# Performance work log

Hardware: AMD Instinct MI355X
Metric: run time of the kernel (lower is better)

Reference implementation:

```python
import jax, jax.numpy as jnp
import numpy as np

H = 12          # num attention heads
D_HEAD = 64     # head size (768 / 12)
P = 2           # power-law exponent
C = 5.0         # score shift
EPS = 1e-10


def setup_inputs() -> dict:
    key = jax.random.key(0)
    ks = jax.random.split(key, 8)
    B, S, Dm = 32, 512, 768
    scale = 1.0 / np.sqrt(Dm)
    return {
        "hidden_states": jax.random.normal(ks[0], (B, S, Dm), dtype=jnp.float32),
        "attention_mask": jnp.ones((B, 1, 1, S), dtype=jnp.float32),
        "Wq": jax.random.normal(ks[1], (Dm, Dm), dtype=jnp.float32) * scale,
        "bq": jnp.zeros((Dm,), dtype=jnp.float32),
        "Wk": jax.random.normal(ks[2], (Dm, Dm), dtype=jnp.float32) * scale,
        "bk": jnp.zeros((Dm,), dtype=jnp.float32),
        "Wv": jax.random.normal(ks[3], (Dm, Dm), dtype=jnp.float32) * scale,
        "bv": jnp.zeros((Dm,), dtype=jnp.float32),
    }


def _heads(x, B, S):
    # [B, S, H*d] -> [B, H, S, d]
    return x.reshape(B, S, H, D_HEAD).transpose(0, 2, 1, 3)


def reference(hidden_states, attention_mask, Wq, bq, Wk, bk, Wv, bv):
    B, S, Dm = hidden_states.shape
    q = _heads(hidden_states @ Wq + bq, B, S)
    k = _heads(hidden_states @ Wk + bk, B, S)
    v = _heads(hidden_states @ Wv + bv, B, S)

    inv_sqrt_d = 1.0 / (np.sqrt(D_HEAD) + 1e-10)
    scores = jnp.einsum("bhqd,bhkd->bhqk", q, k) * inv_sqrt_d  # [B,H,S,S]

    # Power-law attention (Powerformer, distill=0 branch)
    probs = jnp.power(scores + C, P)
    probs = probs / (jnp.sum(probs, axis=-1, keepdims=True) + EPS)
    probs = probs * attention_mask  # mask multiplied after normalization

    ctx = jnp.einsum("bhqk,bhkd->bhqd", probs, v)  # [B,H,S,d]
    ctx = ctx.transpose(0, 2, 1, 3).reshape(B, S, Dm)
    return ctx
```

## Files before the change

### kernel.cpp

```cpp
#include <hip/hip_runtime.h>

typedef __attribute__((ext_vector_type(8))) _Float16 half8;
typedef __attribute__((ext_vector_type(4))) _Float16 half4;
typedef __attribute__((ext_vector_type(4))) float f32x4;

#define MFMA_K32(a, b, c) __builtin_amdgcn_mfma_f32_16x16x32_f16((a), (b), (c), 0, 0, 0)
#define MFMA_K16(a, b, c) __builtin_amdgcn_mfma_f32_16x16x16f16((a), (b), (c), 0, 0, 0)

__device__ inline void async16(const _Float16* g, _Float16* l) {
    __builtin_amdgcn_global_load_lds(
        (const __attribute__((address_space(1))) void*)g,
        (__attribute__((address_space(3))) void*)l, 16, 0, 0);
}


__global__ __launch_bounds__(256) void prep_kernel(
    const float* __restrict__ X, _Float16* __restrict__ Xh,
    const float* __restrict__ W0, const float* __restrict__ W1,
    const float* __restrict__ W2,
    _Float16* __restrict__ T0, _Float16* __restrict__ T1,
    _Float16* __restrict__ T2)
{
    __shared__ float tile[32][33];
    int bid = blockIdx.x;
    if (bid < 6144) {
        size_t idx = ((size_t)bid * 256 + threadIdx.x) * 8;
        float4 a = *(const float4*)(X + idx);
        float4 c = *(const float4*)(X + idx + 4);
        half8 hv;
        hv[0] = (_Float16)a.x; hv[1] = (_Float16)a.y;
        hv[2] = (_Float16)a.z; hv[3] = (_Float16)a.w;
        hv[4] = (_Float16)c.x; hv[5] = (_Float16)c.y;
        hv[6] = (_Float16)c.z; hv[7] = (_Float16)c.w;
        *(half8*)(Xh + idx) = hv;
    } else {
        int id = bid - 6144;
        int z = id / 576; id -= z * 576;
        int n0 = (id / 24) * 32, k0 = (id % 24) * 32;
        const float* W = (z == 0) ? W0 : (z == 1) ? W1 : W2;
        _Float16* T = (z == 0) ? T0 : (z == 1) ? T1 : T2;
        int tx = threadIdx.x & 31, ty = threadIdx.x >> 5;
#pragma unroll
        for (int r = 0; r < 4; ++r)
            tile[ty + 8 * r][tx] = W[(size_t)(k0 + ty + 8 * r) * 768 + n0 + tx];
        __syncthreads();
#pragma unroll
        for (int r = 0; r < 4; ++r)
            T[(size_t)(n0 + ty + 8 * r) * 768 + k0 + tx] =
                (_Float16)tile[tx][ty + 8 * r];
    }
}

__global__ __launch_bounds__(256) void qkv_gemm(
    const _Float16* __restrict__ Xh,
    const _Float16* __restrict__ W0, const _Float16* __restrict__ W1,
    const _Float16* __restrict__ W2,
    const float* __restrict__ b0, const float* __restrict__ b1,
    const float* __restrict__ b2,
    const float* __restrict__ mask,
    _Float16* __restrict__ Qo, _Float16* __restrict__ Ko,
    _Float16* __restrict__ Vo)
{
    int z = blockIdx.y / 6;
    int n0 = (blockIdx.y % 6) * 128;
    int m0 = blockIdx.x * 128;
    const _Float16* Wt = (z == 0) ? W0 : (z == 1) ? W1 : W2;
    const float* bias = (z == 0) ? b0 : (z == 1) ? b1 : b2;

    __shared__ __attribute__((aligned(16))) _Float16 As[128 * 64];
    __shared__ __attribute__((aligned(16))) _Float16 Bs[128 * 64];

    int t = threadIdx.x;
    int wave = t >> 6, lane = t & 63, quad = lane >> 4, l16 = lane & 15;
    int wm = (wave & 1) * 64, wn = (wave >> 1) * 64;

    int srow = t >> 3;
    int sg = (t & 7) ^ (srow & 7);

    const _Float16* gA = Xh + (size_t)(m0 + srow) * 768 + sg * 8;
    const _Float16* gB = Wt + (size_t)(n0 + srow) * 768 + sg * 8;
    _Float16* lA = As + t * 8;
    _Float16* lB = Bs + t * 8;

    const _Float16* Pa = (z == 2) ? As : Bs;
    const _Float16* Pb = (z == 2) ? Bs : As;

    f32x4 acc[4][4] = {};

    for (int k0 = 0; k0 < 768; k0 += 64) {
#pragma unroll
        for (int q = 0; q < 4; ++q) {
            async16(gA + (size_t)q * 32 * 768 + k0, lA + q * 2048);
            async16(gB + (size_t)q * 32 * 768 + k0, lB + q * 2048);
        }
        __syncthreads();
#pragma unroll
        for (int ks = 0; ks < 2; ++ks) {
            half8 af[4], bf[4];
#pragma unroll
            for (int i = 0; i < 4; ++i) {
                int row = wm + i * 16 + l16;
                af[i] = *(const half8*)&Pa[row * 64 +
                                           (((ks << 2) + quad) ^ (row & 7)) * 8];
            }
#pragma unroll
            for (int j = 0; j < 4; ++j) {
                int row = wn + j * 16 + l16;
                bf[j] = *(const half8*)&Pb[row * 64 +
                                           (((ks << 2) + quad) ^ (row & 7)) * 8];
            }
#pragma unroll
            for (int i = 0; i < 4; ++i)
#pragma unroll
                for (int j = 0; j < 4; ++j)
                    acc[i][j] = MFMA_K32(af[i], bf[j], acc[i][j]);
        }
        __syncthreads();
    }

    if (z != 2) {
#pragma unroll
        for (int i = 0; i < 4; ++i) {
            int nbase = n0 + wm + i * 16 + quad * 4;
            int hh = nbase >> 6, dbase = nbase & 63;
            float4 bv4 = *(const float4*)&bias[nbase];
#pragma unroll
            for (int j = 0; j < 4; ++j) {
                int token = m0 + wn + j * 16 + l16;
                int bb = token >> 9, s = token & 511;
                half4 pk;
                if (z == 0) {
#pragma unroll
                    for (int r = 0; r < 4; ++r)
                        pk[r] = (_Float16)((acc[i][j][r] + ((const float*)&bv4)[r]) * 0.125f);
                } else {
#pragma unroll
                    for (int r = 0; r < 4; ++r)
                        pk[r] = (_Float16)(acc[i][j][r] + ((const float*)&bv4)[r]);
                }
                size_t off = (((size_t)(bb * 12 + hh)) * 512 + s) * 64 + dbase;
                if (z == 0) *(half4*)&Qo[off] = pk;
                else        *(half4*)&Ko[off] = pk;
            }
        }
    } else {
        float mk[4][4];
#pragma unroll
        for (int i = 0; i < 4; ++i) {
            int mbase = m0 + wm + i * 16 + quad * 4;
            int bb = mbase >> 9, s = mbase & 511;
#pragma unroll
            for (int r = 0; r < 4; ++r)
                mk[i][r] = mask[(size_t)bb * 512 + s + r];
        }
#pragma unroll
        for (int j = 0; j < 4; ++j) {
            int n = n0 + wn + j * 16 + l16;
            float bv = bias[n];
            int hh = n >> 6, d = n & 63;
#pragma unroll
            for (int i = 0; i < 4; ++i) {
                int mbase = m0 + wm + i * 16 + quad * 4;
                int bb = mbase >> 9, s = mbase & 511;
                half4 pk;
#pragma unroll
                for (int r = 0; r < 4; ++r)
                    pk[r] = (_Float16)((acc[i][j][r] + bv) * mk[i][r]);
                size_t off = (((size_t)(bb * 12 + hh)) * 64 + d) * 512 + s;
                *(half4*)&Vo[off] = pk;
            }
        }
    }
}

__global__ __launch_bounds__(256) void attn_kernel(
    const _Float16* __restrict__ Q, const _Float16* __restrict__ K,
    const _Float16* __restrict__ Vt, float* __restrict__ out)
{
    __shared__ __attribute__((aligned(16))) _Float16 Ks[2][64 * 88];
    __shared__ __attribute__((aligned(16))) _Float16 Vs[2][64 * 88];

    int t = threadIdx.x;
    int wave = t >> 6, lane = t & 63, quad = lane >> 4, l16 = lane & 15;
    int h = blockIdx.y, b = blockIdx.z;
    size_t bh = (size_t)b * 12 + h;
    const _Float16* Qp = Q + bh * (512 * 64);
    const _Float16* Kp = K + bh * (512 * 64);
    const _Float16* Vp = Vt + bh * (64 * 512);
    int qbase = blockIdx.x * 256 + wave * 64;

    half8 qf[4][2];
#pragma unroll
    for (int i = 0; i < 4; ++i)
#pragma unroll
        for (int ks = 0; ks < 2; ++ks)
            qf[i][ks] = *(const half8*)(Qp + (size_t)(qbase + i * 16 + l16) * 64 +
                                        ks * 32 + quad * 8);

    f32x4 ctx[4][4] = {};
    f32x4 rsum[4] = {};
    const half4 ones = {(_Float16)1.f, (_Float16)1.f, (_Float16)1.f, (_Float16)1.f};

    int srow = t >> 2, spart = (t & 3) * 16;
    const _Float16* kgb = Kp + (size_t)srow * 64 + spart;
    const _Float16* vgb = Vp + (size_t)srow * 512 + spart;

    half8 ka0 = *(const half8*)(kgb);
    half8 ka1 = *(const half8*)(kgb + 8);
    half8 va0 = *(const half8*)(vgb);
    half8 va1 = *(const half8*)(vgb + 8);
    *(half8*)&Ks[0][srow * 88 + spart] = ka0;
    *(half8*)&Ks[0][srow * 88 + spart + 8] = ka1;
    *(half8*)&Vs[0][srow * 88 + spart] = va0;
    *(half8*)&Vs[0][srow * 88 + spart + 8] = va1;
    __syncthreads();

    for (int kt = 0; kt < 8; ++kt) {
        int c = kt & 1;
        if (kt < 7) {
            size_t ko = (size_t)(kt + 1) * 64;
            ka0 = *(const half8*)(kgb + ko * 64);
            ka1 = *(const half8*)(kgb + ko * 64 + 8);
            va0 = *(const half8*)(vgb + ko);
            va1 = *(const half8*)(vgb + ko + 8);
        }

        __builtin_amdgcn_s_setprio(1);
#pragma unroll
        for (int kb = 0; kb < 4; ++kb) {
            half8 kf0 = *(const half8*)&Ks[c][(kb * 16 + l16) * 88 + quad * 8];
            half8 kf1 = *(const half8*)&Ks[c][(kb * 16 + l16) * 88 + 32 + quad * 8];
            f32x4 sc[4];
#pragma unroll
            for (int i = 0; i < 4; ++i) {
                f32x4 s0 = {0.f, 0.f, 0.f, 0.f};
                s0 = MFMA_K32(kf0, qf[i][0], s0);
                sc[i] = MFMA_K32(kf1, qf[i][1], s0);
            }
            half4 pA[4];
#pragma unroll
            for (int i = 0; i < 4; ++i) {
#pragma unroll
                for (int r = 0; r < 4; ++r) {
                    float s = sc[i][r] + 5.0f;
                    pA[i][r] = (_Float16)(s * s);
                }
            }
#pragma unroll
            for (int i = 0; i < 4; ++i)
                rsum[i] = MFMA_K16(pA[i], ones, rsum[i]);
#pragma unroll
            for (int n = 0; n < 4; ++n) {
                half4 vf = *(const half4*)&Vs[c][(n * 16 + l16) * 88 + kb * 16 + quad * 4];
#pragma unroll
                for (int i = 0; i < 4; ++i)
                    ctx[i][n] = MFMA_K16(pA[i], vf, ctx[i][n]);
            }
        }
        __builtin_amdgcn_s_setprio(0);

        if (kt < 7) {
            *(half8*)&Ks[1 - c][srow * 88 + spart] = ka0;
            *(half8*)&Ks[1 - c][srow * 88 + spart + 8] = ka1;
            *(half8*)&Vs[1 - c][srow * 88 + spart] = va0;
            *(half8*)&Vs[1 - c][srow * 88 + spart + 8] = va1;
        }
        __syncthreads();
    }

#pragma unroll
    for (int i = 0; i < 4; ++i) {
        f32x4 inv;
#pragma unroll
        for (int r = 0; r < 4; ++r)
            inv[r] = 1.0f / (rsum[i][r] + 1e-10f);
#pragma unroll
        for (int n = 0; n < 4; ++n)
#pragma unroll
            for (int r = 0; r < 4; ++r) {
                int q = qbase + i * 16 + quad * 4 + r;
                int d = n * 16 + l16;
                out[((size_t)b * 512 + q) * 768 + h * 64 + d] =
                    ctx[i][n][r] * inv[r];
            }
    }
}

extern "C" void kernel_launch(void* const* d_in, const int* in_sizes, int n_in,
                              void* d_out, int out_size, void* d_ws, size_t ws_size,
                              hipStream_t stream)
{
    const float* hs   = (const float*)d_in[0];
    const float* mask = (const float*)d_in[1];
    const float* Wq   = (const float*)d_in[2];
    const float* bq   = (const float*)d_in[3];
    const float* Wk   = (const float*)d_in[4];
    const float* bk   = (const float*)d_in[5];
    const float* Wv   = (const float*)d_in[6];
    const float* bv   = (const float*)d_in[7];
    float* out = (float*)d_out;

    char* ws = (char*)d_ws;
    _Float16* Wtq = (_Float16*)ws;
    _Float16* Wtk = Wtq + 768 * 768;
    _Float16* Wtv = Wtk + 768 * 768;
    _Float16* Qb  = Wtv + 768 * 768;
    _Float16* Kb  = Qb + 16384 * 768;
    _Float16* Vb  = Kb + 16384 * 768;
    _Float16* Xh = (_Float16*)d_out;

    prep_kernel<<<dim3(7872), 256, 0, stream>>>(hs, Xh, Wq, Wk, Wv,
                                                Wtq, Wtk, Wtv);
    qkv_gemm<<<dim3(128, 18), 256, 0, stream>>>(Xh, Wtq, Wtk, Wtv,
                                                bq, bk, bv, mask, Qb, Kb, Vb);
    attn_kernel<<<dim3(2, 12, 32), 256, 0, stream>>>(Qb, Kb, Vb, out);
}
```

Before: 234.1 us.

## Double-buffer QKV GEMM LDS tiles with K=32 steps and async prefetch

Restructures the QKV projection GEMM main loop to use two LDS buffers of 128x32 tiles, issuing async global-to-LDS loads for the next K slice while MFMAs run on the current one. This aims to hide global load latency behind compute and cut one barrier per iteration. It also drops the XOR swizzle in favour of a plain 32-element row layout, which may bring LDS bank conflicts back on the fragment reads. The iteration count doubles to 24 with a smaller K per step.

```diff
diff --git a/kernel.cpp b/kernel.cpp
--- a/kernel.cpp
+++ b/kernel.cpp
@@ -67,56 +67,53 @@
     const _Float16* Wt = (z == 0) ? W0 : (z == 1) ? W1 : W2;
     const float* bias = (z == 0) ? b0 : (z == 1) ? b1 : b2;
 
-    __shared__ __attribute__((aligned(16))) _Float16 As[128 * 64];
-    __shared__ __attribute__((aligned(16))) _Float16 Bs[128 * 64];
+    __shared__ __attribute__((aligned(16))) _Float16 As[2 * 4096];
+    __shared__ __attribute__((aligned(16))) _Float16 Bs[2 * 4096];
 
     int t = threadIdx.x;
     int wave = t >> 6, lane = t & 63, quad = lane >> 4, l16 = lane & 15;
     int wm = (wave & 1) * 64, wn = (wave >> 1) * 64;
 
-    int srow = t >> 3;
-    int sg = (t & 7) ^ (srow & 7);
-
-    const _Float16* gA = Xh + (size_t)(m0 + srow) * 768 + sg * 8;
-    const _Float16* gB = Wt + (size_t)(n0 + srow) * 768 + sg * 8;
+    int tr4 = t >> 2, tc4 = t & 3;
+    const _Float16* gA = Xh + (size_t)(m0 + tr4) * 768 + tc4 * 8;
+    const _Float16* gB = Wt + (size_t)(n0 + tr4) * 768 + tc4 * 8;
     _Float16* lA = As + t * 8;
     _Float16* lB = Bs + t * 8;
 
+#define STAGE(buf, k0v) do {                                          \
+        async16(gA + (k0v),              lA + (buf) * 4096);          \
+        async16(gA + 64 * 768 + (k0v),   lA + (buf) * 4096 + 2048);   \
+        async16(gB + (k0v),              lB + (buf) * 4096);          \
+        async16(gB + 64 * 768 + (k0v),   lB + (buf) * 4096 + 2048); } while (0)
+
     const _Float16* Pa = (z == 2) ? As : Bs;
     const _Float16* Pb = (z == 2) ? Bs : As;
 
     f32x4 acc[4][4] = {};
 
-    for (int k0 = 0; k0 < 768; k0 += 64) {
-#pragma unroll
-        for (int q = 0; q < 4; ++q) {
-            async16(gA + (size_t)q * 32 * 768 + k0, lA + q * 2048);
-            async16(gB + (size_t)q * 32 * 768 + k0, lB + q * 2048);
-        }
+    STAGE(0, 0);
+    __syncthreads();
+
+    for (int kt = 0; kt < 24; ++kt) {
+        int c = kt & 1;
+        if (kt < 23) STAGE(c ^ 1, (kt + 1) * 32);
+
+        half8 af[4], bf[4];
+#pragma unroll
+        for (int i = 0; i < 4; ++i)
+            af[i] = *(const half8*)&Pa[c * 4096 + (wm + i * 16 + l16) * 32 + quad * 8];
+#pragma unroll
+        for (int j = 0; j < 4; ++j)
+            bf[j] = *(const half8*)&Pb[c * 4096 + (wn + j * 16 + l16) * 32 + quad * 8];
+#pragma unroll
+        for (int i = 0; i < 4; ++i)
+#pragma unroll
+            for (int j = 0; j < 4; ++j)
+                acc[i][j] = MFMA_K32(af[i], bf[j], acc[i][j]);
+
         __syncthreads();
-#pragma unroll
-        for (int ks = 0; ks < 2; ++ks) {
-            half8 af[4], bf[4];
-#pragma unroll
-            for (int i = 0; i < 4; ++i) {
-                int row = wm + i * 16 + l16;
-                af[i] = *(const half8*)&Pa[row * 64 +
-                                           (((ks << 2) + quad) ^ (row & 7)) * 8];
-            }
-#pragma unroll
-            for (int j = 0; j < 4; ++j) {
-                int row = wn + j * 16 + l16;
-                bf[j] = *(const half8*)&Pb[row * 64 +
-                                           (((ks << 2) + quad) ^ (row & 7)) * 8];
-            }
-#pragma unroll
-            for (int i = 0; i < 4; ++i)
-#pragma unroll
-                for (int j = 0; j < 4; ++j)
-                    acc[i][j] = MFMA_K32(af[i], bf[j], acc[i][j]);
-        }
-        __syncthreads();
-    }
+    }
+#undef STAGE
 
     if (z != 2) {
 #pragma unroll
```

After: 246.7 us. 1.05x slower.

## Double-buffer QKV GEMM LDS tiles with async prefetch of next k-tile

Applied to the files above, without the earlier changes.

The QKV projection GEMM now keeps two LDS buffers for the A and B tiles and issues the asynchronous global-to-LDS loads for the next k-tile before computing on the current one. It waits with a partial vmcnt so only the current tile's loads must have landed. This is meant to hide global load latency behind the MFMA work. In exchange LDS use doubles to 64 KB per block, which may lower occupancy, and the code relies on hand-placed waitcnt and barrier ordering.

```diff
diff --git a/kernel.cpp b/kernel.cpp
--- a/kernel.cpp
+++ b/kernel.cpp
@@ -67,8 +67,8 @@
     const _Float16* Wt = (z == 0) ? W0 : (z == 1) ? W1 : W2;
     const float* bias = (z == 0) ? b0 : (z == 1) ? b1 : b2;
 
-    __shared__ __attribute__((aligned(16))) _Float16 As[128 * 64];
-    __shared__ __attribute__((aligned(16))) _Float16 Bs[128 * 64];
+    __shared__ __attribute__((aligned(16))) _Float16 As[2 * 8192];
+    __shared__ __attribute__((aligned(16))) _Float16 Bs[2 * 8192];
 
     int t = threadIdx.x;
     int wave = t >> 6, lane = t & 63, quad = lane >> 4, l16 = lane & 15;
@@ -82,32 +82,60 @@
     _Float16* lA = As + t * 8;
     _Float16* lB = Bs + t * 8;
 
+#define STAGE(buf, k0v) do {                                                   \
+        async16(gA,                    lA + (buf) * 8192);                     \
+        async16(gA + (size_t)1 * 32 * 768 + (k0v) - (k0v) + (k0v), lA + (buf) * 8192 + 2048); \
+        async16(gA + (size_t)2 * 32 * 768 + (k0v), lA + (buf) * 8192 + 4096);  \
+        async16(gA + (size_t)3 * 32 * 768 + (k0v), lA + (buf) * 8192 + 6144);  \
+        async16(gB + (k0v),            lB + (buf) * 8192);                     \
+        async16(gB + (size_t)1 * 32 * 768 + (k0v), lB + (buf) * 8192 + 2048);  \
+        async16(gB + (size_t)2 * 32 * 768 + (k0v), lB + (buf) * 8192 + 4096);  \
+        async16(gB + (size_t)3 * 32 * 768 + (k0v), lB + (buf) * 8192 + 6144); } while (0)
+#undef STAGE
+#define STAGE(buf, k0v) do {                                                   \
+        async16(gA + (k0v),                        lA + (buf) * 8192);         \
+        async16(gA + (size_t)1 * 32 * 768 + (k0v), lA + (buf) * 8192 + 2048);  \
+        async16(gA + (size_t)2 * 32 * 768 + (k0v), lA + (buf) * 8192 + 4096);  \
+        async16(gA + (size_t)3 * 32 * 768 + (k0v), lA + (buf) * 8192 + 6144);  \
+        async16(gB + (k0v),                        lB + (buf) * 8192);         \
+        async16(gB + (size_t)1 * 32 * 768 + (k0v), lB + (buf) * 8192 + 2048);  \
+        async16(gB + (size_t)2 * 32 * 768 + (k0v), lB + (buf) * 8192 + 4096);  \
+        async16(gB + (size_t)3 * 32 * 768 + (k0v), lB + (buf) * 8192 + 6144); } while (0)
+
     const _Float16* Pa = (z == 2) ? As : Bs;
     const _Float16* Pb = (z == 2) ? Bs : As;
 
     f32x4 acc[4][4] = {};
 
-    for (int k0 = 0; k0 < 768; k0 += 64) {
-#pragma unroll
-        for (int q = 0; q < 4; ++q) {
-            async16(gA + (size_t)q * 32 * 768 + k0, lA + q * 2048);
-            async16(gB + (size_t)q * 32 * 768 + k0, lB + q * 2048);
-        }
-        __syncthreads();
+    STAGE(0, 0);
+
+    for (int kt = 0; kt < 12; ++kt) {
+        int c = kt & 1;
+        if (kt < 11) {
+            STAGE(c ^ 1, (kt + 1) * 64);
+            asm volatile("s_waitcnt vmcnt(8)" ::: "memory");
+        } else {
+            asm volatile("s_waitcnt vmcnt(0)" ::: "memory");
+        }
+        __builtin_amdgcn_s_barrier();
+        __builtin_amdgcn_sched_barrier(0);
+
+        const _Float16* Pa_ = Pa + c * 8192;
+        const _Float16* Pb_ = Pb + c * 8192;
 #pragma unroll
         for (int ks = 0; ks < 2; ++ks) {
             half8 af[4], bf[4];
 #pragma unroll
             for (int i = 0; i < 4; ++i) {
                 int row = wm + i * 16 + l16;
-                af[i] = *(const half8*)&Pa[row * 64 +
-                                           (((ks << 2) + quad) ^ (row & 7)) * 8];
+                af[i] = *(const half8*)&Pa_[row * 64 +
+                                            (((ks << 2) + quad) ^ (row & 7)) * 8];
             }
 #pragma unroll
             for (int j = 0; j < 4; ++j) {
                 int row = wn + j * 16 + l16;
-                bf[j] = *(const half8*)&Pb[row * 64 +
-                                           (((ks << 2) + quad) ^ (row & 7)) * 8];
+                bf[j] = *(const half8*)&Pb_[row * 64 +
+                                            (((ks << 2) + quad) ^ (row & 7)) * 8];
             }
 #pragma unroll
             for (int i = 0; i < 4; ++i)
@@ -115,8 +143,10 @@
                 for (int j = 0; j < 4; ++j)
                     acc[i][j] = MFMA_K32(af[i], bf[j], acc[i][j]);
         }
-        __syncthreads();
-    }
+        __builtin_amdgcn_sched_barrier(0);
+        __builtin_amdgcn_s_barrier();
+    }
+#undef STAGE
 
     if (z != 2) {
 #pragma unroll
```

Result: slower. 239.5 us (+2.3%).
